# Optimization experiments

Measured on AMD Instinct MI355X. Metric: run time of the kernel, lower is better.

The kernel has to match this reference:

```python
import jax, jax.numpy as jnp
import numpy as np

# static config (matches init_kwargs)
NH, NKV, E, K = 16, 4, 8, 2
CAP_FACTOR = 1.25
LN_EPS = 1e-5


def _layer_norm(x, w, b):
    mu = jnp.mean(x, axis=-1, keepdims=True)
    var = jnp.mean(jnp.square(x - mu), axis=-1, keepdims=True)
    return (x - mu) * jax.lax.rsqrt(var + LN_EPS) * w + b


def setup_inputs() -> dict:
    key = jax.random.key(0)
    ks = jax.random.split(key, 6)
    S, B, H, F = 2048, 1, 1024, 2048
    HD = H // NH
    qkv_out = NKV * ((NH // NKV) + 2) * HD  # 1536
    f32 = jnp.float32
    return {
        "hidden_states": jax.random.normal(ks[0], (S, B, H), f32),
        "ln1_weight": jnp.ones((H,), f32),
        "ln1_bias": jnp.zeros((H,), f32),
        "ln2_weight": jnp.ones((H,), f32),
        "ln2_bias": jnp.zeros((H,), f32),
        "qkv_weight": jax.random.normal(ks[1], (qkv_out, H), f32) * 0.02,
        "proj_weight": jax.random.normal(ks[2], (H, H), f32) * 0.02,
        "router_weight": jax.random.normal(ks[3], (H, E), f32) * 0.02,
        "moe_w1": jax.random.normal(ks[4], (E, H, F), f32) * 0.02,
        "moe_w2": jax.random.normal(ks[5], (F and E, F, H), f32)[:E] * 0.02 if False else jax.random.normal(ks[5], (E, F, H), f32) * 0.02,
    }


def reference(hidden_states, ln1_weight, ln1_bias, ln2_weight, ln2_bias,
              qkv_weight, proj_weight, router_weight, moe_w1, moe_w2):
    S, B, H = hidden_states.shape
    HD = H // NH
    q_per_kv = NH // NKV
    # ---- attention block (cp_size=1: all-to-alls are identity) ----
    ln1 = _layer_norm(hidden_states, ln1_weight, ln1_bias)
    qkv = jnp.einsum('sbh,oh->sbo', ln1, qkv_weight)
    qkv = qkv.reshape(S, B, NKV, (q_per_kv + 2) * HD)
    q = qkv[..., : q_per_kv * HD].reshape(S, B, NH, HD)
    k = qkv[..., q_per_kv * HD:(q_per_kv + 1) * HD]          # [S,B,NKV,HD]
    v = qkv[..., (q_per_kv + 1) * HD:]                        # [S,B,NKV,HD]
    qb = jnp.transpose(q, (1, 2, 0, 3)).reshape(B, NKV, q_per_kv, S, HD)
    kb = jnp.transpose(k, (1, 2, 0, 3))                       # [B,NKV,S,HD]
    vb = jnp.transpose(v, (1, 2, 0, 3))
    scale = 1.0 / np.sqrt(HD).astype(np.float32)
    scores = jnp.einsum('bgqsd,bgtd->bgqst', qb, kb) * scale  # [B,NKV,qpk,S,S]
    causal = jnp.tril(jnp.ones((S, S), bool))
    scores = jnp.where(causal, scores, jnp.finfo(scores.dtype).min)
    attn = jax.nn.softmax(scores, axis=-1)
    ao = jnp.einsum('bgqst,bgtd->bgqsd', attn, vb)
    ao = ao.reshape(B, NH, S, HD)
    ao = jnp.transpose(ao, (2, 0, 1, 3)).reshape(S, B, H)
    proj = jnp.einsum('sbh,oh->sbo', ao, proj_weight)
    h1 = hidden_states + proj
    # ---- MoE block (ep_size=1: uniform all-to-all is identity) ----
    ln2 = _layer_norm(h1, ln2_weight, ln2_bias)
    x = ln2.reshape(-1, H)                                    # [N,H]
    N = x.shape[0]
    logits = x @ router_weight                                # linear(x, router_weight.t())
    probs = jax.nn.softmax(logits, axis=-1)
    top_p, top_i = jax.lax.top_k(probs, K)
    top_p = top_p / jnp.sum(top_p, axis=-1, keepdims=True)
    exp_idx = top_i.reshape(-1)                               # [N*K]
    exp_p = top_p.reshape(-1)
    # stable sort by expert id, capacity-padded dispatch
    order = jnp.argsort(exp_idx, stable=True)
    sorted_exp = exp_idx[order]
    counts = jnp.bincount(exp_idx, length=E)
    offsets = jnp.concatenate([jnp.zeros((1,), counts.dtype), jnp.cumsum(counts)[:-1]])
    within = jnp.arange(N * K) - offsets[sorted_exp]
    cap = int(np.ceil(N * K / E * CAP_FACTOR))
    T = E * cap
    valid = within < cap
    dst = jnp.where(valid, sorted_exp * cap + within, T)      # T = out-of-bounds -> dropped
    padded_tokens = jnp.zeros((T, H), x.dtype).at[dst].set(x[order // K], mode='drop')
    padded_probs = jnp.zeros((T,), exp_p.dtype).at[dst].set(exp_p[order], mode='drop')
    padded_tid = jnp.zeros((T,), jnp.int32).at[dst].set((order // K).astype(jnp.int32), mode='drop')
    # grouped expert GEMMs: [E,cap,H] x [E,H,F] -> gelu -> [E,cap,H]
    xt = padded_tokens.reshape(E, cap, H)
    fc1 = jax.nn.gelu(jnp.einsum('ech,ehf->ecf', xt, moe_w1))
    fc2 = jnp.einsum('ecf,efh->ech', fc1, moe_w2).reshape(T, H)
    weighted = fc2 * padded_probs[:, None]                    # pad slots have prob 0
    moe_out = jnp.zeros((N, H), hidden_states.dtype).at[padded_tid].add(weighted)
    return h1 + moe_out.reshape(S, B, H)
```

## Files before the change

kernel.cpp:

```cpp
#include <hip/hip_runtime.h>
#include <hip/hip_bf16.h>
#include <stdint.h>

#define S_LEN 2048
#define HDIM  1024
#define NHEAD 16
#define NKVH  4
#define HEADD 64
#define QKV_O 1536
#define NEXP  8
#define TOPK  2
#define CAP   640
#define TCAP  (NEXP*CAP)
#define FDIM  2048
#define LOG2E 1.44269504088896f
#define NCHUNK 40

typedef __bf16 bf16x8 __attribute__((ext_vector_type(8)));
typedef float  f32x4  __attribute__((ext_vector_type(4)));
typedef unsigned int u32;
typedef u32 u32x4 __attribute__((ext_vector_type(4)));
typedef unsigned short u16;
typedef u16 u16x8 __attribute__((ext_vector_type(8)));

__device__ __forceinline__ void gload16(const __bf16* g, __bf16* l) {
    __builtin_amdgcn_global_load_lds(
        (const __attribute__((address_space(1))) u32*)g,
        (__attribute__((address_space(3))) u32*)l, 16, 0, 0);
}

__device__ __constant__ const signed char c_strip[NCHUNK] =
    {0,1,2,3, 4,4, 5,5, 6,6, 7,7, 8,8,8, 9,9,9, 10,10,10, 11,11,11,
     12,12,12,12, 13,13,13,13, 14,14,14,14, 15,15,15,15};
__device__ __constant__ const signed char c_chunk[NCHUNK] =
    {0,0,0,0, 0,1, 0,1, 0,1, 0,1, 0,1,2, 0,1,2, 0,1,2, 0,1,2,
     0,1,2,3, 0,1,2,3, 0,1,2,3, 0,1,2,3};
__device__ __constant__ const signed char c_cbase[16] = {0,1,2,3,4,6,8,10,12,15,18,21,24,28,32,36};
__device__ __constant__ const signed char c_nch[16]   = {1,1,1,1,2,2,2,2,3,3,3,3,4,4,4,4};

template<bool BF>
__global__ void ln_kernel(const float* __restrict__ in, const float* __restrict__ w,
                          const float* __restrict__ b, void* __restrict__ outv) {
    int row = blockIdx.x;
    const float* x = in + (size_t)row * HDIM;
    __shared__ float red[256];
    int tid = threadIdx.x;
    float s = 0.f;
    for (int i = tid; i < HDIM; i += 256) s += x[i];
    red[tid] = s; __syncthreads();
    for (int st = 128; st > 0; st >>= 1) { if (tid < st) red[tid] += red[tid+st]; __syncthreads(); }
    float mu = red[0] / HDIM; __syncthreads();
    float v = 0.f;
    for (int i = tid; i < HDIM; i += 256) { float d = x[i]-mu; v += d*d; }
    red[tid] = v; __syncthreads();
    for (int st = 128; st > 0; st >>= 1) { if (tid < st) red[tid] += red[tid+st]; __syncthreads(); }
    float rstd = rsqrtf(red[0]/HDIM + 1e-5f);
    for (int i = tid; i < HDIM; i += 256) {
        float o = (x[i]-mu)*rstd*w[i] + b[i];
        if (BF) ((__bf16*)outv)[(size_t)row*HDIM + i] = (__bf16)o;
        else    ((float*)outv)[(size_t)row*HDIM + i] = o;
    }
}

__global__ void conv_bf16_kernel(const float* __restrict__ src, __bf16* __restrict__ dst, int n8) {
    int i = blockIdx.x*256 + threadIdx.x;
    if (i >= n8) return;
    const float4* s = (const float4*)src + (size_t)i*2;
    float4 a = s[0], b = s[1];
    __bf16 tmp[8] = {(__bf16)a.x,(__bf16)a.y,(__bf16)a.z,(__bf16)a.w,
                     (__bf16)b.x,(__bf16)b.y,(__bf16)b.z,(__bf16)b.w};
    *(u32x4*)(dst + (size_t)i*8) = *(u32x4*)tmp;
}

__global__ __launch_bounds__(256)
void transp_conv_kernel(const float* __restrict__ src, __bf16* __restrict__ dst, int K, int N) {
    __shared__ float t[32][33];
    int e = blockIdx.z;
    src += (size_t)e * K * N;
    dst += (size_t)e * K * N;
    int n0 = blockIdx.x*32, k0 = blockIdx.y*32;
    int tx = threadIdx.x & 31, ty = threadIdx.x >> 5;
    #pragma unroll
    for (int i = 0; i < 32; i += 8)
        t[ty+i][tx] = src[(size_t)(k0+ty+i)*N + n0 + tx];
    __syncthreads();
    #pragma unroll
    for (int i = 0; i < 32; i += 8)
        dst[(size_t)(n0+ty+i)*K + k0 + tx] = (__bf16)t[tx][ty+i];
}

template<int EPI>
__global__ __launch_bounds__(256)
void gemm_bf16_kernel(const __bf16* __restrict__ A, const __bf16* __restrict__ Bt,
                      const float* __restrict__ R, void* __restrict__ Cout,
                      int N, int K, long sA, long sB, long sC) {
    __shared__ __bf16 As[128*64];
    __shared__ __bf16 Bs[128*64];
    const int e = blockIdx.z;
    A  += (size_t)e * sA;
    Bt += (size_t)e * sB;
    const int m0 = blockIdx.y*128, n0 = blockIdx.x*128;
    const int tid = threadIdx.x;
    const int lane = tid & 63, w = tid >> 6;
    const int lr = lane & 15, lg = lane >> 4;
    const int wr = w >> 1, wc = w & 1;
    const int srow8 = lane >> 3, sg = lane & 7;
    f32x4 acc[4][4] = {};
    for (int k0 = 0; k0 < K; k0 += 64) {
        __syncthreads();
        #pragma unroll
        for (int i = 0; i < 4; ++i) {
            int row = 32*w + 8*i + srow8;
            int src_g = sg ^ (row & 7);
            gload16(A  + (size_t)(m0+row)*K + k0 + src_g*8,
                    (__bf16*)((char*)As + (32*w + 8*i)*128));
            gload16(Bt + (size_t)(n0+row)*K + k0 + src_g*8,
                    (__bf16*)((char*)Bs + (32*w + 8*i)*128));
        }
        __syncthreads();
        #pragma unroll
        for (int ks = 0; ks < 2; ++ks) {
            bf16x8 af[4], bfr[4];
            #pragma unroll
            for (int mi = 0; mi < 4; ++mi) {
                int row = wr*64 + mi*16 + lr;
                af[mi] = *(const bf16x8*)((const char*)As + ((row*128 + (lg+4*ks)*16) ^ ((row&7)<<4)));
            }
            #pragma unroll
            for (int ni = 0; ni < 4; ++ni) {
                int row = wc*64 + ni*16 + lr;
                bfr[ni] = *(const bf16x8*)((const char*)Bs + ((row*128 + (lg+4*ks)*16) ^ ((row&7)<<4)));
            }
            #pragma unroll
            for (int mi = 0; mi < 4; ++mi)
                #pragma unroll
                for (int ni = 0; ni < 4; ++ni)
                    acc[mi][ni] = __builtin_amdgcn_mfma_f32_16x16x32_bf16(af[mi], bfr[ni], acc[mi][ni], 0,0,0);
        }
    }
    #pragma unroll
    for (int mi = 0; mi < 4; ++mi) {
        #pragma unroll
        for (int ni = 0; ni < 4; ++ni) {
            #pragma unroll
            for (int r = 0; r < 4; ++r) {
                int row = m0 + wr*64 + mi*16 + lg*4 + r;
                int col = n0 + wc*64 + ni*16 + lr;
                float v = acc[mi][ni][r];
                if (EPI == 1) v += R[(size_t)row*N + col];
                if (EPI == 2) {
                    float t = 0.7978845608028654f * (v + 0.044715f*v*v*v);
                    v = 0.5f * v * (1.f + tanhf(t));
                }
                if (EPI == 2 || EPI == 3)
                    ((__bf16*)Cout)[(size_t)e*sC + (size_t)row*N + col] = (__bf16)v;
                else
                    ((float*)Cout)[(size_t)e*sC + (size_t)row*N + col] = v;
            }
        }
    }
}

__global__ __launch_bounds__(512)
void attn_part_kernel(const __bf16* __restrict__ qkv, float* __restrict__ partO,
                      float* __restrict__ partML) {
    const int cx = blockIdx.x;
    const int h  = blockIdx.y;
    const int hg = h >> 2, qi = h & 3;
    const int qb = c_strip[cx];
    const int t0 = 4 * c_chunk[cx];
    const int t1 = min(qb + 1, t0 + 4);
    const int q0 = qb * 128;
    const int tid  = threadIdx.x;
    const int w    = tid >> 6;
    const int lane = tid & 63;
    const int lr   = lane & 15;
    const int lg   = lane >> 4;

    __shared__ __attribute__((aligned(16))) __bf16 Kls[128*64];
    __shared__ __attribute__((aligned(16))) __bf16 Vls[64*128];
    __shared__ __attribute__((aligned(16))) __bf16 Pls[8][16*128];

    const int krow = tid >> 2, kc = (tid & 3) * 2;
    const int va = tid & 63,  dg  = tid >> 6;
    u32x4 kreg[2]; u16x8 vreg[2];

    const __bf16* kbase = qkv + hg*384 + 256;
    const __bf16* vbase = qkv + hg*384 + 320;

#define ISSUE(T) do { \
        const __bf16* kp = kbase + (size_t)((T)*128 + krow)*QKV_O + kc*8; \
        kreg[0] = *(const u32x4*)(kp); \
        kreg[1] = *(const u32x4*)(kp + 8); \
        const __bf16* vp = vbase + (size_t)((T)*128 + 2*va)*QKV_O + dg*8; \
        vreg[0] = *(const u16x8*)(vp); \
        vreg[1] = *(const u16x8*)(vp + QKV_O); \
    } while(0)

#define COMMIT() do { \
        char* Kb = (char*)Kls; \
        *(u32x4*)(Kb + ((krow*128 + (kc+0)*16) ^ ((krow&7)<<4))) = kreg[0]; \
        *(u32x4*)(Kb + ((krow*128 + (kc+1)*16) ^ ((krow&7)<<4))) = kreg[1]; \
        char* Vb = (char*)Vls; \
        _Pragma("unroll") \
        for (int j = 0; j < 8; ++j) { \
            int d = dg*8 + j; \
            u32 u = ((u32)vreg[1][j] << 16) | vreg[0][j]; \
            *(u32*)(Vb + ((d*256 + va*4) ^ ((d&7)<<4))) = u; \
        } \
    } while(0)

    const int qrow = q0 + w*16 + lr;
    const __bf16* qp = qkv + (size_t)qrow*QKV_O + hg*384 + qi*64;
    bf16x8 qfrag[2];
    #pragma unroll
    for (int ks = 0; ks < 2; ++ks) {
        bf16x8 qr = *(const bf16x8*)(qp + ks*32 + lg*8);
        #pragma unroll
        for (int j = 0; j < 8; ++j) qfrag[ks][j] = (__bf16)((float)qr[j] * 0.125f);
    }
    bf16x8 ones;
    #pragma unroll
    for (int j = 0; j < 8; ++j) ones[j] = (__bf16)1.0f;

    f32x4 oacc[4] = {};
    f32x4 lcol = {};
    float mrow[4] = {-INFINITY,-INFINITY,-INFINITY,-INFINITY};

    ISSUE(t0);
    for (int t = t0; t < t1; ++t) {
        __syncthreads();
        COMMIT();
        if (t+1 < t1) ISSUE(t+1);
        __syncthreads();

        f32x4 sacc[8] = {};
        const char* Kb = (const char*)Kls;
        #pragma unroll
        for (int f = 0; f < 8; ++f) {
            int row = lr + 16*f;
            int swz = (row & 7) << 4;
            #pragma unroll
            for (int ks = 0; ks < 2; ++ks) {
                bf16x8 kf = *(const bf16x8*)(Kb + ((row*128 + (lg*8+32*ks)*2) ^ swz));
                sacc[f] = __builtin_amdgcn_mfma_f32_16x16x32_bf16(qfrag[ks], kf, sacc[f], 0,0,0);
            }
        }
        if (t == qb) {
            #pragma unroll
            for (int f = 0; f < 8; ++f)
                #pragma unroll
                for (int r = 0; r < 4; ++r)
                    if (lr + 16*f > 16*w + 4*lg + r) sacc[f][r] = -INFINITY;
        }
        float tm[4];
        #pragma unroll
        for (int r = 0; r < 4; ++r) {
            float a = fmaxf(fmaxf(sacc[0][r], sacc[1][r]), fmaxf(sacc[2][r], sacc[3][r]));
            float b2 = fmaxf(fmaxf(sacc[4][r], sacc[5][r]), fmaxf(sacc[6][r], sacc[7][r]));
            tm[r] = fmaxf(a, b2);
        }
        #pragma unroll
        for (int msk = 1; msk < 16; msk <<= 1)
            #pragma unroll
            for (int r = 0; r < 4; ++r) tm[r] = fmaxf(tm[r], __shfl_xor(tm[r], msk, 64));
        float corr[4];
        #pragma unroll
        for (int r = 0; r < 4; ++r) {
            float mn = fmaxf(mrow[r], tm[r]);
            corr[r] = exp2f((mrow[r]-mn)*LOG2E);
            mrow[r] = mn;
        }
        #pragma unroll
        for (int f = 0; f < 8; ++f)
            #pragma unroll
            for (int r = 0; r < 4; ++r)
                sacc[f][r] = exp2f((sacc[f][r]-mrow[r])*LOG2E);
        #pragma unroll
        for (int ct = 0; ct < 4; ++ct)
            #pragma unroll
            for (int r = 0; r < 4; ++r) oacc[ct][r] *= corr[r];
        #pragma unroll
        for (int r = 0; r < 4; ++r) lcol[r] *= corr[r];
        char* Pw = (char*)&Pls[w][0];
        #pragma unroll
        for (int f = 0; f < 8; ++f)
            #pragma unroll
            for (int r = 0; r < 4; ++r) {
                int row = 4*lg + r, col = lr + 16*f;
                *(__bf16*)(Pw + ((row*256 + col*2) ^ ((row&7)<<4))) = (__bf16)sacc[f][r];
            }
        const char* Vb = (const char*)Vls;
        bf16x8 pa[4];
        #pragma unroll
        for (int ks = 0; ks < 4; ++ks)
            pa[ks] = *(const bf16x8*)(Pw + ((lr*256 + (lg*8+32*ks)*2) ^ ((lr&7)<<4)));
        #pragma unroll
        for (int ks = 0; ks < 4; ++ks)
            lcol = __builtin_amdgcn_mfma_f32_16x16x32_bf16(pa[ks], ones, lcol, 0,0,0);
        #pragma unroll
        for (int ct = 0; ct < 4; ++ct) {
            int row = lr + 16*ct;
            int swz = (row & 7) << 4;
            #pragma unroll
            for (int ks = 0; ks < 4; ++ks) {
                bf16x8 vf = *(const bf16x8*)(Vb + ((row*256 + (lg*8+32*ks)*2) ^ swz));
                oacc[ct] = __builtin_amdgcn_mfma_f32_16x16x32_bf16(pa[ks], vf, oacc[ct], 0,0,0);
            }
        }
    }
    const int p = h*NCHUNK + cx;
    float* po = partO + (size_t)p * (128*64);
    #pragma unroll
    for (int ct = 0; ct < 4; ++ct)
        #pragma unroll
        for (int r = 0; r < 4; ++r)
            po[(16*w + 4*lg + r)*64 + 16*ct + lr] = oacc[ct][r];
    if (lr == 0) {
        float* pm = partML + (size_t)p * 256;
        #pragma unroll
        for (int r = 0; r < 4; ++r) {
            pm[(16*w + 4*lg + r)*2    ] = mrow[r];
            pm[(16*w + 4*lg + r)*2 + 1] = lcol[r];
        }
    }
#undef ISSUE
#undef COMMIT
}

__global__ __launch_bounds__(256)
void attn_combine_kernel(const float* __restrict__ partO, const float* __restrict__ partML,
                         __bf16* __restrict__ ao) {
    const int rb = blockIdx.x, h = blockIdx.y;
    const int row0 = rb*8;
    const int qb = row0 >> 7;
    const int nc = c_nch[qb], cb = c_cbase[qb];
    const int tid = threadIdx.x;
    const int rl = tid >> 5, d2 = (tid & 31) * 2;
    const int grow = row0 + rl;
    const int srow = grow & 127;
    const int pbase = h*NCHUNK + cb;
    float mv[4], lv[4];
    float M = -INFINITY;
    for (int c = 0; c < nc; ++c) {
        const float* pm = partML + (size_t)(pbase+c)*256 + srow*2;
        mv[c] = pm[0]; lv[c] = pm[1];
        M = fmaxf(M, mv[c]);
    }
    float L = 0.f, a0 = 0.f, a1 = 0.f;
    for (int c = 0; c < nc; ++c) {
        float wc = exp2f((mv[c]-M)*LOG2E);
        L += wc * lv[c];
        const float* po = partO + (size_t)(pbase+c)*(128*64) + srow*64 + d2;
        a0 += wc * po[0];
        a1 += wc * po[1];
    }
    float inv = 1.f / L;
    __bf16 o2[2] = {(__bf16)(a0*inv), (__bf16)(a1*inv)};
    *(u32*)(ao + (size_t)grow*HDIM + h*64 + d2) = *(u32*)o2;
}

__global__ __launch_bounds__(256)
void router_kernel(const float* __restrict__ x, const float* __restrict__ rw,
                   int* __restrict__ expi, float* __restrict__ expp) {
    int t = blockIdx.x, tid = threadIdx.x;
    __shared__ float red[256][8];
    float part[8] = {};
    const float* xr = x + (size_t)t*HDIM;
    for (int i = tid; i < HDIM; i += 256) {
        float xv = xr[i];
        const float* wp = rw + (size_t)i*NEXP;
        #pragma unroll
        for (int e2 = 0; e2 < 8; ++e2) part[e2] += xv * wp[e2];
    }
    #pragma unroll
    for (int e2 = 0; e2 < 8; ++e2) red[tid][e2] = part[e2];
    __syncthreads();
    for (int st = 128; st > 0; st >>= 1) {
        if (tid < st)
            #pragma unroll
            for (int e2 = 0; e2 < 8; ++e2) red[tid][e2] += red[tid+st][e2];
        __syncthreads();
    }
    if (tid == 0) {
        float lg[8];
        #pragma unroll
        for (int e2 = 0; e2 < 8; ++e2) lg[e2] = red[0][e2];
        int i0 = 0;
        for (int e2 = 1; e2 < 8; ++e2) if (lg[e2] > lg[i0]) i0 = e2;
        int i1 = -1;
        for (int e2 = 0; e2 < 8; ++e2) { if (e2 == i0) continue; if (i1 < 0 || lg[e2] > lg[i1]) i1 = e2; }
        float p1 = __expf(lg[i1] - lg[i0]);
        float inv = 1.f / (1.f + p1);
        expi[t*2]   = i0; expi[t*2+1] = i1;
        expp[t*2]   = inv; expp[t*2+1] = p1 * inv;
    }
}

__global__ __launch_bounds__(256)
void dst_fast_kernel(const int* __restrict__ expi, int* __restrict__ dst) {
    __shared__ int hist[256][9];
    const int tid = threadIdx.x;
    int ev[16];
    #pragma unroll
    for (int i = 0; i < 16; i += 4)
        *(int4*)(ev+i) = *(const int4*)(expi + tid*16 + i);
    int cnt[8] = {};
    #pragma unroll
    for (int i = 0; i < 16; ++i)
        #pragma unroll
        for (int e = 0; e < 8; ++e) cnt[e] += (ev[i] == e);
    #pragma unroll
    for (int e = 0; e < 8; ++e) hist[tid][e] = cnt[e];
    __syncthreads();
    const int w = tid >> 6, lane = tid & 63;
    #pragma unroll
    for (int rep = 0; rep < 2; ++rep) {
        int e = w + rep*4;
        int h0 = hist[4*lane+0][e], h1 = hist[4*lane+1][e],
            h2 = hist[4*lane+2][e], h3 = hist[4*lane+3][e];
        int s = h0+h1+h2+h3, inc = s;
        #pragma unroll
        for (int off = 1; off < 64; off <<= 1) {
            int v = __shfl_up(inc, off, 64);
            if (lane >= off) inc += v;
        }
        int excl = inc - s;
        hist[4*lane+0][e] = excl;
        hist[4*lane+1][e] = excl + h0;
        hist[4*lane+2][e] = excl + h0 + h1;
        hist[4*lane+3][e] = excl + h0 + h1 + h2;
    }
    __syncthreads();
    int run[8];
    #pragma unroll
    for (int e = 0; e < 8; ++e) run[e] = hist[tid][e];
    int out[16];
    #pragma unroll
    for (int i = 0; i < 16; ++i) {
        int e = ev[i], within = 0;
        #pragma unroll
        for (int e2 = 0; e2 < 8; ++e2)
            if (e == e2) { within = run[e2]; run[e2]++; }
        out[i] = (within < CAP) ? (e*CAP + within) : -1;
    }
    #pragma unroll
    for (int i = 0; i < 16; i += 4)
        *(int4*)(dst + tid*16 + i) = *(const int4*)(out+i);
}

__global__ void scatter_kernel(const float* __restrict__ x, const int* __restrict__ dst,
                               __bf16* __restrict__ xt) {
    int s = blockIdx.x;
    int d = dst[s];
    if (d < 0) return;
    int t = s >> 1;
    int i = threadIdx.x;
    float4 f = ((const float4*)(x + (size_t)t*HDIM))[i];
    __bf16* dp = xt + (size_t)d*HDIM + i*4;
    dp[0]=(__bf16)f.x; dp[1]=(__bf16)f.y; dp[2]=(__bf16)f.z; dp[3]=(__bf16)f.w;
}

__global__ void combine_kernel(const float* __restrict__ h1, const float* __restrict__ fc2,
                               const int* __restrict__ dst, const float* __restrict__ expp,
                               float* __restrict__ out) {
    int t = blockIdx.x;
    int d0 = dst[t*2], d1 = dst[t*2+1];
    float p0 = expp[t*2], p1 = expp[t*2+1];
    for (int i = threadIdx.x; i < HDIM; i += 256) {
        float v = h1[(size_t)t*HDIM + i];
        if (d0 >= 0) v += p0 * fc2[(size_t)d0*HDIM + i];
        if (d1 >= 0) v += p1 * fc2[(size_t)d1*HDIM + i];
        out[(size_t)t*HDIM + i] = v;
    }
}

extern "C" void kernel_launch(void* const* d_in, const int* in_sizes, int n_in,
                              void* d_out, int out_size, void* d_ws, size_t ws_size,
                              hipStream_t stream) {
    const float* hidden = (const float*)d_in[0];
    const float* ln1w   = (const float*)d_in[1];
    const float* ln1b_  = (const float*)d_in[2];
    const float* ln2w   = (const float*)d_in[3];
    const float* ln2b_  = (const float*)d_in[4];
    const float* qkvW   = (const float*)d_in[5];
    const float* projW  = (const float*)d_in[6];
    const float* routW  = (const float*)d_in[7];
    const float* w1     = (const float*)d_in[8];
    const float* w2     = (const float*)d_in[9];
    float* out = (float*)d_out;

    char* base = (char*)d_ws;
    __bf16* w1t    = (__bf16*)(base);
    __bf16* w2t    = (__bf16*)(base + 33554432);
    __bf16* ln1b   = (__bf16*)(base + 0);
    __bf16* qkvWb  = (__bf16*)(base + 4194304);
    __bf16* qkvb   = (__bf16*)(base + 7340032);
    __bf16* aob    = (__bf16*)(base + 13631488);
    __bf16* projWb = (__bf16*)(base + 17825792);
    char* B0 = base + 67108864;
    float*  h1   = (float*)(B0);
    __bf16* xtb  = (__bf16*)(B0 + 8388608);
    __bf16* fc1b = (__bf16*)(B0 + 18874368);
    float*  fc2  = (float*)(B0 + 39845888);
    float*  x2   = fc2;
    int*    expi = (int*)(B0 + 60817408);
    int*    dsts = (int*)(B0 + 60833792);
    float*  expp = (float*)(B0 + 60850176);
    float*  partML = (float*)xtb;
    float*  partO  = (float*)fc1b;

    ln_kernel<true><<<S_LEN, 256, 0, stream>>>(hidden, ln1w, ln1b_, ln1b);
    conv_bf16_kernel<<<(QKV_O*HDIM/8 + 255)/256, 256, 0, stream>>>(qkvW, qkvWb, QKV_O*HDIM/8);
    gemm_bf16_kernel<3><<<dim3(QKV_O/128, S_LEN/128, 1), 256, 0, stream>>>(
        ln1b, qkvWb, nullptr, qkvb, QKV_O, HDIM, 0, 0, 0);
    attn_part_kernel<<<dim3(NCHUNK, NHEAD), 512, 0, stream>>>(qkvb, partO, partML);
    attn_combine_kernel<<<dim3(S_LEN/8, NHEAD), 256, 0, stream>>>(partO, partML, aob);
    conv_bf16_kernel<<<(HDIM*HDIM/8 + 255)/256, 256, 0, stream>>>(projW, projWb, HDIM*HDIM/8);
    gemm_bf16_kernel<1><<<dim3(HDIM/128, S_LEN/128, 1), 256, 0, stream>>>(
        aob, projWb, hidden, h1, HDIM, HDIM, 0, 0, 0);
    ln_kernel<false><<<S_LEN, 256, 0, stream>>>(h1, ln2w, ln2b_, x2);
    router_kernel<<<S_LEN, 256, 0, stream>>>(x2, routW, expi, expp);
    dst_fast_kernel<<<1, 256, 0, stream>>>(expi, dsts);
    hipMemsetAsync(xtb, 0, (size_t)TCAP * HDIM * sizeof(__bf16), stream);
    scatter_kernel<<<S_LEN*TOPK, 256, 0, stream>>>(x2, dsts, xtb);
    transp_conv_kernel<<<dim3(FDIM/32, HDIM/32, NEXP), 256, 0, stream>>>(w1, w1t, HDIM, FDIM);
    transp_conv_kernel<<<dim3(HDIM/32, FDIM/32, NEXP), 256, 0, stream>>>(w2, w2t, FDIM, HDIM);
    gemm_bf16_kernel<2><<<dim3(FDIM/128, CAP/128, NEXP), 256, 0, stream>>>(
        xtb, w1t, nullptr, fc1b, FDIM, HDIM,
        (long)CAP*HDIM, (long)FDIM*HDIM, (long)CAP*FDIM);
    gemm_bf16_kernel<0><<<dim3(HDIM/128, CAP/128, NEXP), 256, 0, stream>>>(
        fc1b, w2t, nullptr, fc2, HDIM, FDIM,
        (long)CAP*FDIM, (long)FDIM*HDIM, (long)CAP*HDIM);
    combine_kernel<<<S_LEN, 256, 0, stream>>>(h1, fc2, dsts, expp, out);
}
```

Measured before the change: 270.1 us.

## Fuse LN1 with weight casts, LN2 with router, and merge expert transposes

LN1 and the bf16 casts of the QKV and projection weights now run in one launch, selected by block index. LN2 is fused into the router kernel, which writes the normalised activations as bf16 so the scatter becomes a plain 8-byte copy. The two expert-weight transposes are merged into one launch, and the memset of the padded expert token buffer is removed. This cuts launch count, memory traffic and the zero-fill. Unfilled pad rows now hold stale data, which is safe only because the combine step never reads dropped slots.

```diff
diff --git a/kernel.cpp b/kernel.cpp
--- a/kernel.cpp
+++ b/kernel.cpp
@@ -20,6 +20,7 @@
 typedef float  f32x4  __attribute__((ext_vector_type(4)));
 typedef unsigned int u32;
 typedef u32 u32x4 __attribute__((ext_vector_type(4)));
+typedef u32 u32x2 __attribute__((ext_vector_type(2)));
 typedef unsigned short u16;
 typedef u16 u16x8 __attribute__((ext_vector_type(8)));
 
@@ -38,47 +39,54 @@
 __device__ __constant__ const signed char c_cbase[16] = {0,1,2,3,4,6,8,10,12,15,18,21,24,28,32,36};
 __device__ __constant__ const signed char c_nch[16]   = {1,1,1,1,2,2,2,2,3,3,3,3,4,4,4,4};
 
-template<bool BF>
-__global__ void ln_kernel(const float* __restrict__ in, const float* __restrict__ w,
-                          const float* __restrict__ b, void* __restrict__ outv) {
-    int row = blockIdx.x;
-    const float* x = in + (size_t)row * HDIM;
-    __shared__ float red[256];
-    int tid = threadIdx.x;
-    float s = 0.f;
-    for (int i = tid; i < HDIM; i += 256) s += x[i];
-    red[tid] = s; __syncthreads();
-    for (int st = 128; st > 0; st >>= 1) { if (tid < st) red[tid] += red[tid+st]; __syncthreads(); }
-    float mu = red[0] / HDIM; __syncthreads();
-    float v = 0.f;
-    for (int i = tid; i < HDIM; i += 256) { float d = x[i]-mu; v += d*d; }
-    red[tid] = v; __syncthreads();
-    for (int st = 128; st > 0; st >>= 1) { if (tid < st) red[tid] += red[tid+st]; __syncthreads(); }
-    float rstd = rsqrtf(red[0]/HDIM + 1e-5f);
-    for (int i = tid; i < HDIM; i += 256) {
-        float o = (x[i]-mu)*rstd*w[i] + b[i];
-        if (BF) ((__bf16*)outv)[(size_t)row*HDIM + i] = (__bf16)o;
-        else    ((float*)outv)[(size_t)row*HDIM + i] = o;
-    }
-}
-
-__global__ void conv_bf16_kernel(const float* __restrict__ src, __bf16* __restrict__ dst, int n8) {
-    int i = blockIdx.x*256 + threadIdx.x;
-    if (i >= n8) return;
+__global__ __launch_bounds__(256)
+void prep_kernel(const float* __restrict__ hidden, const float* __restrict__ ln1w,
+                 const float* __restrict__ ln1bb, const float* __restrict__ qkvW,
+                 const float* __restrict__ projW, __bf16* __restrict__ ln1o,
+                 __bf16* __restrict__ qkvWb, __bf16* __restrict__ projWb) {
+    const int b = blockIdx.x, tid = threadIdx.x;
+    if (b < S_LEN) {
+        __shared__ float red[256];
+        const float* x = hidden + (size_t)b * HDIM;
+        float s = 0.f;
+        for (int i = tid; i < HDIM; i += 256) s += x[i];
+        red[tid] = s; __syncthreads();
+        for (int st = 128; st > 0; st >>= 1) { if (tid < st) red[tid] += red[tid+st]; __syncthreads(); }
+        float mu = red[0] / HDIM; __syncthreads();
+        float v = 0.f;
+        for (int i = tid; i < HDIM; i += 256) { float d = x[i]-mu; v += d*d; }
+        red[tid] = v; __syncthreads();
+        for (int st = 128; st > 0; st >>= 1) { if (tid < st) red[tid] += red[tid+st]; __syncthreads(); }
+        float rstd = rsqrtf(red[0]/HDIM + 1e-5f);
+        for (int i = tid; i < HDIM; i += 256)
+            ln1o[(size_t)b*HDIM + i] = (__bf16)((x[i]-mu)*rstd*ln1w[i] + ln1bb[i]);
+        return;
+    }
+    const float* src; __bf16* dst; int i;
+    if (b < S_LEN + 768) { src = qkvW; dst = qkvWb; i = (b - S_LEN)*256 + tid; }
+    else                 { src = projW; dst = projWb; i = (b - S_LEN - 768)*256 + tid; }
     const float4* s = (const float4*)src + (size_t)i*2;
-    float4 a = s[0], b = s[1];
+    float4 a = s[0], b4 = s[1];
     __bf16 tmp[8] = {(__bf16)a.x,(__bf16)a.y,(__bf16)a.z,(__bf16)a.w,
-                     (__bf16)b.x,(__bf16)b.y,(__bf16)b.z,(__bf16)b.w};
+                     (__bf16)b4.x,(__bf16)b4.y,(__bf16)b4.z,(__bf16)b4.w};
     *(u32x4*)(dst + (size_t)i*8) = *(u32x4*)tmp;
 }
 
 __global__ __launch_bounds__(256)
-void transp_conv_kernel(const float* __restrict__ src, __bf16* __restrict__ dst, int K, int N) {
+void transp2_kernel(const float* __restrict__ w1, const float* __restrict__ w2,
+                    __bf16* __restrict__ w1t, __bf16* __restrict__ w2t) {
     __shared__ float t[32][33];
-    int e = blockIdx.z;
-    src += (size_t)e * K * N;
-    dst += (size_t)e * K * N;
-    int n0 = blockIdx.x*32, k0 = blockIdx.y*32;
+    const int b = blockIdx.x;
+    const float* src; __bf16* dst; int K, N, n0, k0, e;
+    if (b < 16384) {
+        e = b >> 11; int rem = b & 2047;
+        K = HDIM; N = FDIM; n0 = (rem & 63) * 32; k0 = (rem >> 6) * 32;
+        src = w1 + (size_t)e*K*N; dst = w1t + (size_t)e*K*N;
+    } else {
+        int bb = b - 16384; e = bb >> 11; int rem = bb & 2047;
+        K = FDIM; N = HDIM; n0 = (rem & 31) * 32; k0 = (rem >> 5) * 32;
+        src = w2 + (size_t)e*K*N; dst = w2t + (size_t)e*K*N;
+    }
     int tx = threadIdx.x & 31, ty = threadIdx.x >> 5;
     #pragma unroll
     for (int i = 0; i < 32; i += 8)
@@ -361,31 +369,45 @@
 }
 
 __global__ __launch_bounds__(256)
-void router_kernel(const float* __restrict__ x, const float* __restrict__ rw,
-                   int* __restrict__ expi, float* __restrict__ expp) {
-    int t = blockIdx.x, tid = threadIdx.x;
-    __shared__ float red[256][8];
+void ln2_router_kernel(const float* __restrict__ h1, const float* __restrict__ w,
+                       const float* __restrict__ b, const float* __restrict__ rw,
+                       __bf16* __restrict__ x2b, int* __restrict__ expi,
+                       float* __restrict__ expp) {
+    const int t = blockIdx.x, tid = threadIdx.x;
+    __shared__ float red[256];
+    __shared__ float red8[256][8];
+    const float* x = h1 + (size_t)t*HDIM;
+    float s = 0.f;
+    for (int i = tid; i < HDIM; i += 256) s += x[i];
+    red[tid] = s; __syncthreads();
+    for (int st = 128; st > 0; st >>= 1) { if (tid < st) red[tid] += red[tid+st]; __syncthreads(); }
+    float mu = red[0] / HDIM; __syncthreads();
+    float v = 0.f;
+    for (int i = tid; i < HDIM; i += 256) { float d = x[i]-mu; v += d*d; }
+    red[tid] = v; __syncthreads();
+    for (int st = 128; st > 0; st >>= 1) { if (tid < st) red[tid] += red[tid+st]; __syncthreads(); }
+    float rstd = rsqrtf(red[0]/HDIM + 1e-5f);
     float part[8] = {};
-    const float* xr = x + (size_t)t*HDIM;
     for (int i = tid; i < HDIM; i += 256) {
-        float xv = xr[i];
+        float o = (x[i]-mu)*rstd*w[i] + b[i];
+        x2b[(size_t)t*HDIM + i] = (__bf16)o;
         const float* wp = rw + (size_t)i*NEXP;
         #pragma unroll
-        for (int e2 = 0; e2 < 8; ++e2) part[e2] += xv * wp[e2];
-    }
-    #pragma unroll
-    for (int e2 = 0; e2 < 8; ++e2) red[tid][e2] = part[e2];
+        for (int e2 = 0; e2 < 8; ++e2) part[e2] += o * wp[e2];
+    }
+    #pragma unroll
+    for (int e2 = 0; e2 < 8; ++e2) red8[tid][e2] = part[e2];
     __syncthreads();
     for (int st = 128; st > 0; st >>= 1) {
         if (tid < st)
             #pragma unroll
-            for (int e2 = 0; e2 < 8; ++e2) red[tid][e2] += red[tid+st][e2];
+            for (int e2 = 0; e2 < 8; ++e2) red8[tid][e2] += red8[tid+st][e2];
         __syncthreads();
     }
     if (tid == 0) {
         float lg[8];
         #pragma unroll
-        for (int e2 = 0; e2 < 8; ++e2) lg[e2] = red[0][e2];
+        for (int e2 = 0; e2 < 8; ++e2) lg[e2] = red8[0][e2];
         int i0 = 0;
         for (int e2 = 1; e2 < 8; ++e2) if (lg[e2] > lg[i0]) i0 = e2;
         int i1 = -1;
@@ -449,16 +471,15 @@
         *(int4*)(dst + tid*16 + i) = *(const int4*)(out+i);
 }
 
-__global__ void scatter_kernel(const float* __restrict__ x, const int* __restrict__ dst,
+__global__ void scatter_kernel(const __bf16* __restrict__ x2b, const int* __restrict__ dst,
                                __bf16* __restrict__ xt) {
     int s = blockIdx.x;
     int d = dst[s];
     if (d < 0) return;
     int t = s >> 1;
     int i = threadIdx.x;
-    float4 f = ((const float4*)(x + (size_t)t*HDIM))[i];
-    __bf16* dp = xt + (size_t)d*HDIM + i*4;
-    dp[0]=(__bf16)f.x; dp[1]=(__bf16)f.y; dp[2]=(__bf16)f.z; dp[3]=(__bf16)f.w;
+    u32x2 v = *(const u32x2*)(x2b + (size_t)t*HDIM + i*4);
+    *(u32x2*)(xt + (size_t)d*HDIM + i*4) = v;
 }
 
 __global__ void combine_kernel(const float* __restrict__ h1, const float* __restrict__ fc2,
@@ -503,29 +524,25 @@
     __bf16* xtb  = (__bf16*)(B0 + 8388608);
     __bf16* fc1b = (__bf16*)(B0 + 18874368);
     float*  fc2  = (float*)(B0 + 39845888);
-    float*  x2   = fc2;
+    __bf16* x2b  = (__bf16*)fc2;
     int*    expi = (int*)(B0 + 60817408);
     int*    dsts = (int*)(B0 + 60833792);
     float*  expp = (float*)(B0 + 60850176);
     float*  partML = (float*)xtb;
     float*  partO  = (float*)fc1b;
 
-    ln_kernel<true><<<S_LEN, 256, 0, stream>>>(hidden, ln1w, ln1b_, ln1b);
-    conv_bf16_kernel<<<(QKV_O*HDIM/8 + 255)/256, 256, 0, stream>>>(qkvW, qkvWb, QKV_O*HDIM/8);
+    prep_kernel<<<S_LEN + 768 + 512, 256, 0, stream>>>(
+        hidden, ln1w, ln1b_, qkvW, projW, ln1b, qkvWb, projWb);
     gemm_bf16_kernel<3><<<dim3(QKV_O/128, S_LEN/128, 1), 256, 0, stream>>>(
         ln1b, qkvWb, nullptr, qkvb, QKV_O, HDIM, 0, 0, 0);
     attn_part_kernel<<<dim3(NCHUNK, NHEAD), 512, 0, stream>>>(qkvb, partO, partML);
     attn_combine_kernel<<<dim3(S_LEN/8, NHEAD), 256, 0, stream>>>(partO, partML, aob);
-    conv_bf16_kernel<<<(HDIM*HDIM/8 + 255)/256, 256, 0, stream>>>(projW, projWb, HDIM*HDIM/8);
     gemm_bf16_kernel<1><<<dim3(HDIM/128, S_LEN/128, 1), 256, 0, stream>>>(
         aob, projWb, hidden, h1, HDIM, HDIM, 0, 0, 0);
-    ln_kernel<false><<<S_LEN, 256, 0, stream>>>(h1, ln2w, ln2b_, x2);
-    router_kernel<<<S_LEN, 256, 0, stream>>>(x2, routW, expi, expp);
+    ln2_router_kernel<<<S_LEN, 256, 0, stream>>>(h1, ln2w, ln2b_, routW, x2b, expi, expp);
     dst_fast_kernel<<<1, 256, 0, stream>>>(expi, dsts);
-    hipMemsetAsync(xtb, 0, (size_t)TCAP * HDIM * sizeof(__bf16), stream);
-    scatter_kernel<<<S_LEN*TOPK, 256, 0, stream>>>(x2, dsts, xtb);
-    transp_conv_kernel<<<dim3(FDIM/32, HDIM/32, NEXP), 256, 0, stream>>>(w1, w1t, HDIM, FDIM);
-    transp_conv_kernel<<<dim3(HDIM/32, FDIM/32, NEXP), 256, 0, stream>>>(w2, w2t, FDIM, HDIM);
+    scatter_kernel<<<S_LEN*TOPK, 256, 0, stream>>>(x2b, dsts, xtb);
+    transp2_kernel<<<32768, 256, 0, stream>>>(w1, w2, w1t, w2t);
     gemm_bf16_kernel<2><<<dim3(FDIM/128, CAP/128, NEXP), 256, 0, stream>>>(
         xtb, w1t, nullptr, fc1b, FDIM, HDIM,
         (long)CAP*HDIM, (long)FDIM*HDIM, (long)CAP*FDIM);
```

New measurement: 255.7 us. -5.3%, faster.
